# Kernel optimization log

Hardware: AMD Instinct MI355X
Metric: run time of the kernel (lower is better)

Reference implementation:

```python
import jax, jax.numpy as jnp
import numpy as np
import math

NUM_HEADS = 8

def setup_inputs() -> dict:
    key = jax.random.key(0)
    k1, k2, k3 = jax.random.split(key, 3)
    B, N, C = 16, 4096, 512
    x = jax.random.normal(k1, (B, N, C), dtype=jnp.float32)
    qkv_w = jax.random.normal(k2, (3 * C, C), dtype=jnp.float32) * 0.02
    proj_w = jax.random.normal(k3, (C, C), dtype=jnp.float32) * 0.02
    proj_b = jnp.zeros((C,), dtype=jnp.float32)
    return {"x": x, "qkv_w": qkv_w, "proj_w": proj_w, "proj_b": proj_b}


def reference(x, qkv_w, proj_w, proj_b):
    # Attention with is_mask=1: row-wise windowed attention.
    B, N, C = x.shape
    H = W = int(math.isqrt(N))
    nh = NUM_HEADS
    hd = C // nh
    scale = hd ** (-0.5)

    # fold rows into batch: (B*H, W, C)
    img = x.reshape(B * H, W, C)
    # qkv linear (no bias): (B*H, W, 3C) -> (3, B*H, nh, W, hd)
    qkv = jnp.einsum('bwc,dc->bwd', img, qkv_w)
    qkv = qkv.reshape(B * H, W, 3, nh, hd).transpose(2, 0, 3, 1, 4)
    q, k, v = qkv[0], qkv[1], qkv[2]

    # scaled dot-product attention within each row window
    attn = jnp.einsum('bhqd,bhkd->bhqk', q, k) * scale
    attn = jax.nn.softmax(attn, axis=-1)
    out = jnp.einsum('bhqk,bhkd->bhqd', attn, v)   # (B*H, nh, W, hd)
    out = out.transpose(0, 2, 1, 3).reshape(B, N, C)

    # output projection
    return jnp.einsum('bnc,dc->bnd', out, proj_w) + proj_b
```

## Files before the change

### kernel.cpp

```cpp
#include <hip/hip_runtime.h>
#include <cstdint>
#include <cstddef>

typedef _Float16 half8 __attribute__((ext_vector_type(8)));
typedef _Float16 half4 __attribute__((ext_vector_type(4)));
typedef float f32x4 __attribute__((ext_vector_type(4)));

#define GLDS16(g, l) __builtin_amdgcn_global_load_lds( \
    (__attribute__((address_space(1))) void*)(g), \
    (__attribute__((address_space(3))) void*)(l), 16, 0, 0)

#define LBAR() do { asm volatile("s_waitcnt lgkmcnt(0)" ::: "memory"); \
                    __builtin_amdgcn_s_barrier(); } while (0)

#define PH_MID() do { __builtin_amdgcn_sched_barrier(0); \
                      __builtin_amdgcn_s_barrier(); \
                      __builtin_amdgcn_sched_barrier(0); \
                      __builtin_amdgcn_s_setprio(1); } while (0)
#define PH_END() do { __builtin_amdgcn_s_setprio(0); \
                      __builtin_amdgcn_sched_barrier(0); \
                      __builtin_amdgcn_s_barrier(); } while (0)

__global__ __launch_bounds__(256) void cvt_f32_f16(const float* __restrict__ src,
                                                   _Float16* __restrict__ dst, int n) {
  int i = (blockIdx.x * 256 + threadIdx.x) * 8;
  if (i >= n) return;
  float4 a = *(const float4*)(src + i);
  float4 b = *(const float4*)(src + i + 4);
  half8 h;
  h[0] = (_Float16)a.x; h[1] = (_Float16)a.y; h[2] = (_Float16)a.z; h[3] = (_Float16)a.w;
  h[4] = (_Float16)b.x; h[5] = (_Float16)b.y; h[6] = (_Float16)b.z; h[7] = (_Float16)b.w;
  *(half8*)(dst + i) = h;
}

template<int NOUT, int NT, bool BIAS>
__global__ __launch_bounds__(512, 2) void gemm_bt(const _Float16* __restrict__ A,
                                                  const _Float16* __restrict__ Bw,
                                                  const float* __restrict__ bias,
                                                  void* __restrict__ Cout) {
  constexpr int K = 512;
  __shared__ union {
    _Float16 S[2][2][16384];
    float E[2][16][264];
  } u;
  const int id  = blockIdx.x;
  const int xcd = id & 7;
  const int jj  = id >> 3;
  const int by  = (jj / NT) * 8 + xcd;
  const int bx  = jj % NT;
  const int m_base = by * 256, n_base = bx * 256;

  const int t    = threadIdx.x;
  const int lane = t & 63;
  const int wid  = t >> 6;
  const int wm   = wid & 1;
  const int wn   = wid >> 1;
  const int cl   = lane & 15, q = lane >> 4;

  f32x4 acc[8][4] = {};

  const int r0 = ((t >> 7) << 4) | (t & 15);
  const int c0 = (t >> 4) & 7;
  const _Float16* aR = A  + (size_t)(m_base + r0) * K + c0 * 8;
  const _Float16* bR = Bw + (size_t)(n_base + r0) * K + c0 * 8;
  char* Sb = (char*)&u.S[0][0][0];

  auto stageA = [&](int p, int h, int kt) {
    char* dst = Sb + p * 65536 + h * 16384 + t * 16;
    const _Float16* s = aR + (size_t)(h * 128) * K + kt * 64;
    GLDS16(s, dst);
    GLDS16(s + (size_t)64 * K, dst + 8192);
  };
  auto stageB = [&](int p, int h, int kt) {
    char* dst = Sb + p * 65536 + 32768 + h * 16384 + t * 16;
    const _Float16* s = bR + (size_t)(h * 128) * K + kt * 64;
    GLDS16(s, dst);
    GLDS16(s + (size_t)64 * K, dst + 8192);
  };

#define QUAD(AM, BN, BF) \
  _Pragma("unroll") for (int i_ = 0; i_ < 4; ++i_) \
  _Pragma("unroll") for (int j_ = 0; j_ < 2; ++j_) \
  _Pragma("unroll") for (int kk_ = 0; kk_ < 2; ++kk_) \
    acc[(AM)*4 + i_][(BN)*2 + j_] = __builtin_amdgcn_mfma_f32_16x16x32_f16( \
        af[i_][kk_], BF[j_][kk_], acc[(AM)*4 + i_][(BN)*2 + j_], 0, 0, 0);

  stageA(0, 0, 0); stageA(0, 1, 0); stageB(0, 0, 0); stageB(0, 1, 0);
  stageB(1, 0, 1); stageB(1, 1, 1);
  asm volatile("s_waitcnt vmcnt(4)" ::: "memory");
  __builtin_amdgcn_s_barrier();

  half8 af[4][2], bf0[2][2], bf1[2][2];
#pragma unroll
  for (int c = 0; c < 8; ++c) {
    const int p = c & 1;
    const char* aB = (const char*)u.S[p][0] + wm * 16384 + lane * 16;
    const char* bB = (const char*)u.S[p][1] + wn * 8192 + lane * 16;

#pragma unroll
    for (int fm = 0; fm < 4; ++fm)
#pragma unroll
      for (int kk = 0; kk < 2; ++kk)
        af[fm][kk] = *(const half8*)(aB + fm * 2048 + kk * 1024);
#pragma unroll
    for (int fn = 0; fn < 2; ++fn)
#pragma unroll
      for (int kk = 0; kk < 2; ++kk)
        bf0[fn][kk] = *(const half8*)(bB + fn * 2048 + kk * 1024);
    if (c + 1 < 8) stageA(p ^ 1, 0, c + 1);
    PH_MID();
    QUAD(0, 0, bf0);
    PH_END();

#pragma unroll
    for (int fn = 0; fn < 2; ++fn)
#pragma unroll
      for (int kk = 0; kk < 2; ++kk)
        bf1[fn][kk] = *(const half8*)(bB + (2 + fn) * 2048 + kk * 1024);
    if (c + 1 < 8) stageA(p ^ 1, 1, c + 1);
    PH_MID();
    QUAD(0, 1, bf1);
    PH_END();

#pragma unroll
    for (int fm = 0; fm < 4; ++fm)
#pragma unroll
      for (int kk = 0; kk < 2; ++kk)
        af[fm][kk] = *(const half8*)(aB + (4 + fm) * 2048 + kk * 1024);
    if (c + 2 < 8) stageB(p, 0, c + 2);
    PH_MID();
    QUAD(1, 1, bf1);
    PH_END();

    if (c + 2 < 8) stageB(p, 1, c + 2);
    PH_MID();
    QUAD(1, 0, bf0);
    __builtin_amdgcn_s_setprio(0);
    __builtin_amdgcn_sched_barrier(0);
    if (c < 6)       { asm volatile("s_waitcnt vmcnt(4)" ::: "memory"); }
    else if (c == 6) { asm volatile("s_waitcnt vmcnt(0)" ::: "memory"); }
    __builtin_amdgcn_s_barrier();
  }
#undef QUAD

  const int eb = t >> 8;
  const int erow = (t >> 4) & 15;
  const int ecs = t & 15;
#pragma unroll
  for (int j = 0; j < 8; ++j) {
#pragma unroll
    for (int nt = 0; nt < 4; nt++)
#pragma unroll
      for (int r = 0; r < 4; r++)
        u.E[wm][q * 4 + r][wn * 64 + nt * 16 + cl] = acc[j][nt][r];
    LBAR();
    const size_t rg = (size_t)(m_base + (eb * 8 + j) * 16 + erow);
#pragma unroll
    for (int jo = 0; jo < 4; jo++) {
      const int cc = (ecs + 16 * jo) * 4;
      float4 e = *(const float4*)&u.E[eb][erow][cc];
      if constexpr (BIAS) {
        const float4 bb = *(const float4*)(bias + n_base + cc);
        e.x += bb.x; e.y += bb.y; e.z += bb.z; e.w += bb.w;
        *(float4*)((float*)Cout + rg * NOUT + n_base + cc) = e;
      } else {
        half4 hv;
        hv[0] = (_Float16)e.x; hv[1] = (_Float16)e.y;
        hv[2] = (_Float16)e.z; hv[3] = (_Float16)e.w;
        *(half4*)((_Float16*)Cout + rg * NOUT + n_base + cc) = hv;
      }
    }
    LBAR();
  }
}

__global__ __launch_bounds__(256, 3) void attn_win(const _Float16* __restrict__ QKV,
                                                   _Float16* __restrict__ Out) {
  __shared__ _Float16 Qs[4096];
  __shared__ _Float16 Ks[4096];
  __shared__ _Float16 Vt[64][72];
  __shared__ _Float16 Ps[64][72];
  __shared__ _Float16 Os[64][72];
  const int h = blockIdx.x, b = blockIdx.y;
  const int t = threadIdx.x;
  const int lane = t & 63, wid = t >> 6;
  const int cl = lane & 15, q = lane >> 4;

  {
    const int s0 = t, s1 = t + 256;
    const int r0 = ((s0 >> 7) << 4) | (s0 & 15), ch0 = (s0 >> 4) & 7;
    const int r1 = ((s1 >> 7) << 4) | (s1 & 15), ch1 = (s1 >> 4) & 7;
    const _Float16* g0 = QKV + (size_t)(b * 64 + r0) * 1536 + h * 64 + ch0 * 8;
    const _Float16* g1 = QKV + (size_t)(b * 64 + r1) * 1536 + h * 64 + ch1 * 8;
    GLDS16(g0,       (char*)Qs + s0 * 16);
    GLDS16(g1,       (char*)Qs + s1 * 16);
    GLDS16(g0 + 512, (char*)Ks + s0 * 16);
    GLDS16(g1 + 512, (char*)Ks + s1 * 16);

    const int vj = t & 63, vp = t >> 6;
    const _Float16* vsrc = QKV + (size_t)(b * 64 + vj) * 1536 + 1024 + h * 64 + vp * 16;
    half8 v0 = *(const half8*)vsrc;
    half8 v1 = *(const half8*)(vsrc + 8);
#pragma unroll
    for (int i = 0; i < 8; i++) Vt[vp * 16 + i][vj] = v0[i];
#pragma unroll
    for (int i = 0; i < 8; i++) Vt[vp * 16 + 8 + i][vj] = v1[i];
  }
  __syncthreads();

  const int m0 = wid * 16;
  const int lane8 = lane * 8;

  f32x4 s[4] = {};
#pragma unroll
  for (int ks = 0; ks < 2; ks++) {
    half8 a = *(const half8*)(Qs + wid * 1024 + ks * 512 + lane8);
#pragma unroll
    for (int nt = 0; nt < 4; nt++) {
      half8 bb = *(const half8*)(Ks + nt * 1024 + ks * 512 + lane8);
      s[nt] = __builtin_amdgcn_mfma_f32_16x16x32_f16(a, bb, s[nt], 0, 0, 0);
    }
  }

  constexpr float SC = 0.125f * 1.44269504088896340736f;
#pragma unroll
  for (int r = 0; r < 4; r++) {
    float mx = fmaxf(fmaxf(s[0][r], s[1][r]), fmaxf(s[2][r], s[3][r]));
    mx = fmaxf(mx, __shfl_xor(mx, 1));
    mx = fmaxf(mx, __shfl_xor(mx, 2));
    mx = fmaxf(mx, __shfl_xor(mx, 4));
    mx = fmaxf(mx, __shfl_xor(mx, 8));
    float e[4], ssum = 0.f;
#pragma unroll
    for (int nt = 0; nt < 4; nt++) { e[nt] = exp2f((s[nt][r] - mx) * SC); ssum += e[nt]; }
    ssum += __shfl_xor(ssum, 1);
    ssum += __shfl_xor(ssum, 2);
    ssum += __shfl_xor(ssum, 4);
    ssum += __shfl_xor(ssum, 8);
    float inv = 1.f / ssum;
    const int row = m0 + q * 4 + r;
#pragma unroll
    for (int nt = 0; nt < 4; nt++) Ps[row][nt * 16 + cl] = (_Float16)(e[nt] * inv);
  }
  __syncthreads();

  f32x4 o[4] = {};
#pragma unroll
  for (int ks = 0; ks < 2; ks++) {
    half8 a = *(const half8*)&Ps[m0 + cl][ks * 32 + q * 8];
#pragma unroll
    for (int nt = 0; nt < 4; nt++) {
      half8 bb = *(const half8*)&Vt[nt * 16 + cl][ks * 32 + q * 8];
      o[nt] = __builtin_amdgcn_mfma_f32_16x16x32_f16(a, bb, o[nt], 0, 0, 0);
    }
  }
#pragma unroll
  for (int nt = 0; nt < 4; nt++)
#pragma unroll
    for (int r = 0; r < 4; r++)
      Os[m0 + q * 4 + r][nt * 16 + cl] = (_Float16)o[nt][r];
  __syncthreads();

  {
    const int row = t >> 2, cs = t & 3;
    half8 h0 = *(const half8*)&Os[row][cs * 16];
    half8 h1 = *(const half8*)&Os[row][cs * 16 + 8];
    _Float16* dst = Out + (size_t)(b * 64 + row) * 512 + h * 64 + cs * 16;
    *(half8*)dst = h0;
    *((half8*)dst + 1) = h1;
  }
}

extern "C" void kernel_launch(void* const* d_in, const int* in_sizes, int n_in,
                              void* d_out, int out_size, void* d_ws, size_t ws_size,
                              hipStream_t stream) {
  const float* x      = (const float*)d_in[0];
  const float* qkv_w  = (const float*)d_in[1];
  const float* proj_w = (const float*)d_in[2];
  const float* proj_b = (const float*)d_in[3];
  float* out = (float*)d_out;

  char* ws = (char*)d_ws;
  _Float16* QKVh = (_Float16*)ws;
  _Float16* Xh   = (_Float16*)(ws + 201326592);
  _Float16* Outh = Xh;
  _Float16* Wq   = (_Float16*)(ws + 268435456);
  _Float16* Wp   = (_Float16*)(ws + 270008320);

  cvt_f32_f16<<<16384, 256, 0, stream>>>(x, Xh, 16 * 4096 * 512);
  cvt_f32_f16<<<384, 256, 0, stream>>>(qkv_w, Wq, 1536 * 512);
  cvt_f32_f16<<<128, 256, 0, stream>>>(proj_w, Wp, 512 * 512);
  gemm_bt<1536, 6, false><<<1536, 512, 0, stream>>>(Xh, Wq, nullptr, QKVh);
  attn_win<<<dim3(8, 1024), 256, 0, stream>>>(QKVh, Outh);
  gemm_bt<512, 2, true><<<512, 512, 0, stream>>>(Outh, Wp, proj_b, out);
}
```

Before: 481.1 us.

## Add smaller-tile projection GEMM and slim attention LDS usage

Adds a 128x128-tile, 256-thread GEMM variant with a double-buffered LDS pipeline and uses it for the output projection, so that GEMM runs as more, smaller blocks across the GPU. The attention kernel now loads Q straight into registers and writes O directly to global memory, dropping the Qs and Os LDS buffers and one barrier so more blocks fit per CU (launch bounds raised to 5). In exchange, the direct O stores are scalar 2-byte writes rather than coalesced 16-byte ones, and the projection GEMM's smaller tiles reuse each loaded tile less.

```diff
diff --git a/kernel.cpp b/kernel.cpp
--- a/kernel.cpp
+++ b/kernel.cpp
@@ -174,28 +174,130 @@
   }
 }
 
-__global__ __launch_bounds__(256, 3) void attn_win(const _Float16* __restrict__ QKV,
+template<int NOUT, int NT, bool BIAS>
+__global__ __launch_bounds__(256, 2) void gemm_bt_s(const _Float16* __restrict__ A,
+                                                    const _Float16* __restrict__ Bw,
+                                                    const float* __restrict__ bias,
+                                                    void* __restrict__ Cout) {
+  constexpr int K = 512;
+  constexpr int NIT = K / 64;
+  __shared__ union {
+    _Float16 S[2][2][8192];
+    float E[2][16][132];
+  } u;
+  const int id  = blockIdx.x;
+  const int xcd = id & 7;
+  const int jj  = id >> 3;
+  const int by  = (jj / NT) * 8 + xcd;
+  const int bx  = jj % NT;
+  const int m_base = by * 128, n_base = bx * 128;
+
+  const int t    = threadIdx.x;
+  const int lane = t & 63;
+  const int wid  = t >> 6;
+  const int wm   = wid >> 1, wn = wid & 1;
+  const int cl   = lane & 15, q = lane >> 4;
+
+  f32x4 acc[4][4] = {};
+
+  const _Float16* aP[4];
+  const _Float16* bP[4];
+#pragma unroll
+  for (int i = 0; i < 4; ++i) {
+    const int s = t + i * 256;
+    const int r = ((s >> 7) << 4) | (s & 15), ch = (s >> 4) & 7;
+    aP[i] = A  + (size_t)(m_base + r) * K + ch * 8;
+    bP[i] = Bw + (size_t)(n_base + r) * K + ch * 8;
+  }
+  auto stage = [&](int kt) {
+    const int p = kt & 1;
+    const int ko = kt * 64;
+#pragma unroll
+    for (int i = 0; i < 4; ++i) {
+      GLDS16(aP[i] + ko, (char*)&u.S[p][0][0] + (t + i * 256) * 16);
+      GLDS16(bP[i] + ko, (char*)&u.S[p][1][0] + (t + i * 256) * 16);
+    }
+  };
+
+  stage(0);
+#pragma unroll
+  for (int k = 0; k < NIT; ++k) {
+    if (k + 1 < NIT) { stage(k + 1); asm volatile("s_waitcnt vmcnt(8)" ::: "memory"); }
+    else             { asm volatile("s_waitcnt vmcnt(0)" ::: "memory"); }
+    __builtin_amdgcn_s_barrier();
+    asm volatile("" ::: "memory");
+
+    const _Float16* As = &u.S[k & 1][0][0];
+    const _Float16* Bs = &u.S[k & 1][1][0];
+    half8 af[4][2], bf[4][2];
+#pragma unroll
+    for (int i = 0; i < 4; i++)
+#pragma unroll
+      for (int kk = 0; kk < 2; kk++) {
+        af[i][kk] = *(const half8*)(As + (wm * 4 + i) * 1024 + kk * 512 + lane * 8);
+        bf[i][kk] = *(const half8*)(Bs + (wn * 4 + i) * 1024 + kk * 512 + lane * 8);
+      }
+#pragma unroll
+    for (int mt = 0; mt < 4; mt++)
+#pragma unroll
+      for (int nt = 0; nt < 4; nt++)
+#pragma unroll
+        for (int kk = 0; kk < 2; kk++)
+          acc[mt][nt] = __builtin_amdgcn_mfma_f32_16x16x32_f16(af[mt][kk], bf[nt][kk],
+                                                               acc[mt][nt], 0, 0, 0);
+    __builtin_amdgcn_s_barrier();
+  }
+
+  const int ebnd = t >> 7, erow = (t >> 3) & 15, ecs = t & 7;
+#pragma unroll
+  for (int mt = 0; mt < 4; mt++) {
+#pragma unroll
+    for (int nt = 0; nt < 4; nt++)
+#pragma unroll
+      for (int r = 0; r < 4; r++)
+        u.E[wm][q * 4 + r][wn * 64 + nt * 16 + cl] = acc[mt][nt][r];
+    LBAR();
+    const size_t rg = (size_t)(m_base + ebnd * 64 + mt * 16 + erow);
+#pragma unroll
+    for (int j = 0; j < 4; j++) {
+      const int ch = ((ecs - erow) & 7) + 8 * j;
+      const int cc = ch * 4;
+      float4 e = *(const float4*)&u.E[ebnd][erow][cc];
+      if constexpr (BIAS) {
+        const float4 bb = *(const float4*)(bias + n_base + cc);
+        e.x += bb.x; e.y += bb.y; e.z += bb.z; e.w += bb.w;
+        *(float4*)((float*)Cout + rg * NOUT + n_base + cc) = e;
+      } else {
+        half4 hv;
+        hv[0] = (_Float16)e.x; hv[1] = (_Float16)e.y;
+        hv[2] = (_Float16)e.z; hv[3] = (_Float16)e.w;
+        *(half4*)((_Float16*)Cout + rg * NOUT + n_base + cc) = hv;
+      }
+    }
+    LBAR();
+  }
+}
+
+__global__ __launch_bounds__(256, 5) void attn_win(const _Float16* __restrict__ QKV,
                                                    _Float16* __restrict__ Out) {
-  __shared__ _Float16 Qs[4096];
   __shared__ _Float16 Ks[4096];
   __shared__ _Float16 Vt[64][72];
   __shared__ _Float16 Ps[64][72];
-  __shared__ _Float16 Os[64][72];
   const int h = blockIdx.x, b = blockIdx.y;
   const int t = threadIdx.x;
   const int lane = t & 63, wid = t >> 6;
   const int cl = lane & 15, q = lane >> 4;
+  const int m0 = wid * 16;
+  const int lane8 = lane * 8;
 
   {
     const int s0 = t, s1 = t + 256;
     const int r0 = ((s0 >> 7) << 4) | (s0 & 15), ch0 = (s0 >> 4) & 7;
     const int r1 = ((s1 >> 7) << 4) | (s1 & 15), ch1 = (s1 >> 4) & 7;
-    const _Float16* g0 = QKV + (size_t)(b * 64 + r0) * 1536 + h * 64 + ch0 * 8;
-    const _Float16* g1 = QKV + (size_t)(b * 64 + r1) * 1536 + h * 64 + ch1 * 8;
-    GLDS16(g0,       (char*)Qs + s0 * 16);
-    GLDS16(g1,       (char*)Qs + s1 * 16);
-    GLDS16(g0 + 512, (char*)Ks + s0 * 16);
-    GLDS16(g1 + 512, (char*)Ks + s1 * 16);
+    const _Float16* g0 = QKV + (size_t)(b * 64 + r0) * 1536 + 512 + h * 64 + ch0 * 8;
+    const _Float16* g1 = QKV + (size_t)(b * 64 + r1) * 1536 + 512 + h * 64 + ch1 * 8;
+    GLDS16(g0, (char*)Ks + s0 * 16);
+    GLDS16(g1, (char*)Ks + s1 * 16);
 
     const int vj = t & 63, vp = t >> 6;
     const _Float16* vsrc = QKV + (size_t)(b * 64 + vj) * 1536 + 1024 + h * 64 + vp * 16;
@@ -206,20 +308,20 @@
 #pragma unroll
     for (int i = 0; i < 8; i++) Vt[vp * 16 + 8 + i][vj] = v1[i];
   }
+
+  const _Float16* qsrc = QKV + (size_t)(b * 64 + m0 + cl) * 1536 + h * 64 + q * 8;
+  half8 qa0 = *(const half8*)qsrc;
+  half8 qa1 = *(const half8*)(qsrc + 32);
+
   __syncthreads();
 
-  const int m0 = wid * 16;
-  const int lane8 = lane * 8;
-
   f32x4 s[4] = {};
 #pragma unroll
-  for (int ks = 0; ks < 2; ks++) {
-    half8 a = *(const half8*)(Qs + wid * 1024 + ks * 512 + lane8);
-#pragma unroll
-    for (int nt = 0; nt < 4; nt++) {
-      half8 bb = *(const half8*)(Ks + nt * 1024 + ks * 512 + lane8);
-      s[nt] = __builtin_amdgcn_mfma_f32_16x16x32_f16(a, bb, s[nt], 0, 0, 0);
-    }
+  for (int nt = 0; nt < 4; nt++) {
+    half8 b0 = *(const half8*)(Ks + nt * 1024 + lane8);
+    half8 b1 = *(const half8*)(Ks + nt * 1024 + 512 + lane8);
+    s[nt] = __builtin_amdgcn_mfma_f32_16x16x32_f16(qa0, b0, s[nt], 0, 0, 0);
+    s[nt] = __builtin_amdgcn_mfma_f32_16x16x32_f16(qa1, b1, s[nt], 0, 0, 0);
   }
 
   constexpr float SC = 0.125f * 1.44269504088896340736f;
@@ -254,21 +356,13 @@
       o[nt] = __builtin_amdgcn_mfma_f32_16x16x32_f16(a, bb, o[nt], 0, 0, 0);
     }
   }
+
 #pragma unroll
   for (int nt = 0; nt < 4; nt++)
 #pragma unroll
     for (int r = 0; r < 4; r++)
-      Os[m0 + q * 4 + r][nt * 16 + cl] = (_Float16)o[nt][r];
-  __syncthreads();
-
-  {
-    const int row = t >> 2, cs = t & 3;
-    half8 h0 = *(const half8*)&Os[row][cs * 16];
-    half8 h1 = *(const half8*)&Os[row][cs * 16 + 8];
-    _Float16* dst = Out + (size_t)(b * 64 + row) * 512 + h * 64 + cs * 16;
-    *(half8*)dst = h0;
-    *((half8*)dst + 1) = h1;
-  }
+      Out[(size_t)(b * 64 + m0 + q * 4 + r) * 512 + h * 64 + nt * 16 + cl] =
+          (_Float16)o[nt][r];
 }
 
 extern "C" void kernel_launch(void* const* d_in, const int* in_sizes, int n_in,
@@ -292,5 +386,5 @@
   cvt_f32_f16<<<128, 256, 0, stream>>>(proj_w, Wp, 512 * 512);
   gemm_bt<1536, 6, false><<<1536, 512, 0, stream>>>(Xh, Wq, nullptr, QKVh);
   attn_win<<<dim3(8, 1024), 256, 0, stream>>>(QKVh, Outh);
-  gemm_bt<512, 2, true><<<512, 512, 0, stream>>>(Outh, Wp, proj_b, out);
-}
+  gemm_bt_s<512, 4, true><<<2048, 256, 0, stream>>>(Outh, Wp, proj_b, out);
+}
```

New measurement: 487.4 us. Within noise of the previous version (+1.3%).
